# Kernel tuning notes

Measured on AMD Instinct MI355X. Metric: run time of the kernel, lower is better.

## Reference

```python
import jax, jax.numpy as jnp
import numpy as np

NUM_VARS = 50
EDGE_TYPES = 4
N_HID = 256
MSG_HID = N_HID // 8  # 32
IN_SIZE = 16
BATCH = 512
SKIP_FIRST = True

_adj = np.ones((NUM_VARS, NUM_VARS)) - np.eye(NUM_VARS)
SEND_EDGES, RECV_EDGES = np.where(_adj)
NUM_EDGES = SEND_EDGES.shape[0]  # 2450


def _lin(key, fan_in, fan_out):
    k1, k2 = jax.random.split(key)
    bound = 1.0 / np.sqrt(fan_in)
    w = jax.random.uniform(k1, (fan_in, fan_out), jnp.float32, -bound, bound)
    b = jax.random.uniform(k2, (fan_out,), jnp.float32, -bound, bound)
    return w, b


def setup_inputs() -> dict:
    key = jax.random.key(0)
    ks = jax.random.split(key, 10)
    inputs = jax.random.normal(ks[0], (BATCH, NUM_VARS, IN_SIZE), jnp.float32)
    edges = jax.random.uniform(ks[1], (BATCH, NUM_EDGES, EDGE_TYPES), jnp.float32)
    # per-edge-type message MLPs, stacked over edge-type axis
    f1 = [_lin(jax.random.fold_in(ks[2], i), 2 * IN_SIZE, MSG_HID) for i in range(EDGE_TYPES)]
    f2 = [_lin(jax.random.fold_in(ks[3], i), MSG_HID, MSG_HID) for i in range(EDGE_TYPES)]
    msg_fc1_w = jnp.stack([w for w, _ in f1]); msg_fc1_b = jnp.stack([b for _, b in f1])
    msg_fc2_w = jnp.stack([w for w, _ in f2]); msg_fc2_b = jnp.stack([b for _, b in f2])
    out_fc1_w, out_fc1_b = _lin(ks[4], IN_SIZE + MSG_HID, N_HID)
    out_fc2_w, out_fc2_b = _lin(ks[5], N_HID, N_HID)
    mu_w, mu_b = _lin(ks[6], N_HID, IN_SIZE)
    return dict(inputs=inputs, edges=edges,
                msg_fc1_w=msg_fc1_w, msg_fc1_b=msg_fc1_b,
                msg_fc2_w=msg_fc2_w, msg_fc2_b=msg_fc2_b,
                out_fc1_w=out_fc1_w, out_fc1_b=out_fc1_b,
                out_fc2_w=out_fc2_w, out_fc2_b=out_fc2_b,
                mu_w=mu_w, mu_b=mu_b)


def reference(inputs, edges, msg_fc1_w, msg_fc1_b, msg_fc2_w, msg_fc2_b,
              out_fc1_w, out_fc1_b, out_fc2_w, out_fc2_b, mu_w, mu_b):
    send = jnp.asarray(SEND_EDGES)
    recv = jnp.asarray(RECV_EDGES)
    # gather endpoints: [B, E, 2*in]
    pre_msg = jnp.concatenate([inputs[:, recv, :], inputs[:, send, :]], axis=-1)
    B = inputs.shape[0]
    all_msgs = jnp.zeros((B, NUM_EDGES, MSG_HID), inputs.dtype)
    start = 1 if SKIP_FIRST else 0
    for k in range(start, EDGE_TYPES):  # small fixed loop over edge types
        m = jax.nn.relu(pre_msg @ msg_fc1_w[k] + msg_fc1_b[k])
        m = jax.nn.relu(m @ msg_fc2_w[k] + msg_fc2_b[k])
        all_msgs = all_msgs + m * edges[:, :, k:k + 1]
    # scatter-sum edges -> receiver nodes (replaces dense edge2node_mat matmul)
    agg = jax.ops.segment_sum(jnp.swapaxes(all_msgs, 0, 1), recv,
                              num_segments=NUM_VARS)  # [V, B, H]
    agg = jnp.swapaxes(agg, 0, 1)  # [B, V, H]
    aug = jnp.concatenate([inputs, agg], axis=-1)
    pred = jax.nn.relu(aug @ out_fc1_w + out_fc1_b)
    pred = jax.nn.relu(pred @ out_fc2_w + out_fc2_b)
    mu = pred @ mu_w + mu_b  # eval mode: pi_action = mu (no rsample, dropout p=0)
    return (mu, pred)
```

## Files before the change

kernel.cpp:

```cpp
#include <hip/hip_runtime.h>
#include <hip/hip_bf16.h>
#include <hip/hip_fp16.h>

#define BATCHN 512
#define NV 50
#define NE 2450
#define INSZ 16
#define MH 32
#define NH 256

typedef short s16x8 __attribute__((ext_vector_type(8)));
typedef _Float16 f16x8 __attribute__((ext_vector_type(8)));
typedef float f32x4 __attribute__((ext_vector_type(4)));
typedef float f32x2 __attribute__((ext_vector_type(2)));

#define PRED_OFF (BATCHN * NV * INSZ)


__device__ __forceinline__ unsigned short f2bf(float x) {
  unsigned int u = __float_as_uint(x);
  unsigned int r = (u + 0x7fffu + ((u >> 16) & 1u)) >> 16;
  return (unsigned short)r;
}
__device__ __forceinline__ unsigned short f2h(float x) {
  return __half_as_ushort(__float2half(x));
}
__device__ __forceinline__ unsigned int pk2(float a, float b) {
  return (unsigned int)f2bf(a) | ((unsigned int)f2bf(b) << 16);
}
__device__ __forceinline__ unsigned int cvtpk(float lo, float hi) {
  unsigned int r;
  asm("v_cvt_pk_bf16_f32 %0, %1, %2" : "=v"(r) : "v"(lo), "v"(hi));
  return r;
}
__device__ __forceinline__ unsigned int pkmax0(unsigned int x, unsigned int z) {
  unsigned int r;
  asm("v_pk_max_i16 %0, %1, %2" : "=v"(r) : "v"(x), "v"(z));
  return r;
}
__device__ __forceinline__ unsigned int pkaddh(unsigned int a, unsigned int b) {
  unsigned int r;
  asm("v_pk_add_f16 %0, %1, %2" : "=v"(r) : "v"(a), "v"(b));
  return r;
}
__device__ __forceinline__ void pkfma(f32x2& acc, f32x2 a, f32x2 b) {
  asm("v_pk_fma_f32 %0, %1, %2, %0" : "+v"(acc) : "v"(a), "v"(b));
}

__global__ void k_tr(const float* __restrict__ w1, const float* __restrict__ w2,
                     const float* __restrict__ wo1, const float* __restrict__ wo2,
                     const float* __restrict__ wmu,
                     unsigned short* __restrict__ W2t, unsigned short* __restrict__ W1t,
                     unsigned short* __restrict__ Wt1sw, unsigned short* __restrict__ Wt2sw,
                     unsigned short* __restrict__ Wtmusw) {
  int idx = blockIdx.x * 256 + threadIdx.x;
  if (idx < 3072) {
    int c = idx & 31, h = (idx >> 5) & 31, kk = idx >> 10;
    W2t[idx] = f2h(w2[((kk + 1) * 32 + c) * 32 + h]);
  } else if (idx < 9216) {
    int j = idx - 3072;
    int k = j & 31, n = (j >> 5) & 31, kk = (j >> 10) % 3, half = j / 3072;
    W1t[j] = f2bf(k < 16 ? w1[((kk + 1) * 32 + half * 16 + k) * 32 + n] : 0.f);
  } else if (idx < 9216 + 16384) {
    int j = idx - 9216; int n = j & 255, kl = j >> 8;
    float v = kl < 48 ? wo1[kl * 256 + n] : 0.f;
    Wt1sw[n * 64 + (kl ^ ((n & 7) << 3))] = f2bf(v);
  } else if (idx < 9216 + 16384 + 65536) {
    int j = idx - (9216 + 16384);
    int c = j >> 14, r = j & 16383;
    int n = r & 255, kl = r >> 8;
    float v = wo2[(c * 64 + kl) * 256 + n];
    Wt2sw[(c * 256 + n) * 64 + (kl ^ ((n & 7) << 3))] = f2bf(v);
  } else if (idx < 9216 + 16384 + 65536 + 4096) {
    int j = idx - (9216 + 16384 + 65536);
    int n = j & 15, kl = j >> 4;
    Wtmusw[n * 256 + (kl ^ ((n & 7) << 3))] = f2bf(wmu[kl * 16 + n]);
  }
}

__global__ void __launch_bounds__(512, 4)
k_all(const float* __restrict__ inputs, const float* __restrict__ edges,
      const float* __restrict__ b1, const float* __restrict__ b2,
      const unsigned short* __restrict__ W1t, const unsigned short* __restrict__ W2t,
      const unsigned short* __restrict__ Wt1sw, const float* __restrict__ bo1,
      const unsigned short* __restrict__ Wt2sw, const float* __restrict__ bo2,
      const unsigned short* __restrict__ Wtmusw, const float* __restrict__ bmu,
      float* __restrict__ out) {
  __shared__ __align__(16) char smem[75776];
  unsigned short* S16 = (unsigned short*)(smem);
  unsigned short* R16 = (unsigned short*)(smem + 10400);
  float* E_lds = (float*)(smem + 20800);
  float* comb  = (float*)(smem + 10400);
  float* agg_l = (float*)(smem + 20800);
  unsigned short* aug = (unsigned short*)(smem);
  unsigned short* P1  = (unsigned short*)(smem + 9216);
  unsigned short* WB  = (unsigned short*)(smem + 43008);

  const int b   = blockIdx.x;
  const int tid = threadIdx.x;
  const int w   = tid >> 6;
  const int l   = tid & 63;
  const int grp = l >> 4;
  const int lm  = l & 15;
  const int jt  = w & 3;
  const int ih  = w >> 2;

  for (int x = tid; x < NV * 56; x += 512) {
    int i  = x / 56;
    int js = x - i * 56;
    float4 ev = make_float4(0.f, 0.f, 0.f, 0.f);
    if (js < NV && js != i) {
      int e = i * 49 + js - (js > i ? 1 : 0);
      ev = reinterpret_cast<const float4*>(edges)[b * NE + e];
    }
    int base = i * 168 + js;
    E_lds[base]       = ev.y;
    E_lds[base + 56]  = ev.z;
    E_lds[base + 112] = ev.w;
  }

  {
    const int half = w >> 2;
    const int mt4  = w & 3;
    int node  = mt4 * 16 + lm;
    int nodec = node < NV ? node : NV - 1;
    s16x8 af = {0, 0, 0, 0, 0, 0, 0, 0};
    if (grp < 2) {
      const float4* ip = reinterpret_cast<const float4*>(inputs) + (b * NV + nodec) * 4 + grp * 2;
      float4 x0 = ip[0], x1 = ip[1];
      union { unsigned int u[4]; s16x8 v; } U;
      U.u[0] = cvtpk(x0.x, x0.y); U.u[1] = cvtpk(x0.z, x0.w);
      U.u[2] = cvtpk(x1.x, x1.y); U.u[3] = cvtpk(x1.z, x1.w);
      af = U.v;
    }
    unsigned short* dst = half ? S16 : R16;
#pragma unroll
    for (int kk = 0; kk < 3; ++kk) {
#pragma unroll
      for (int nt = 0; nt < 2; ++nt) {
        int h = lm + 16 * nt;
        s16x8 bf = *reinterpret_cast<const s16x8*>(W1t + ((half * 3 + kk) * 32 + h) * 32 + grp * 8);
        f32x4 C;
        if (half == 0) { float bv = b1[(kk + 1) * 32 + h]; C = f32x4{bv, bv, bv, bv}; }
        else C = f32x4{0.f, 0.f, 0.f, 0.f};
        f32x4 o = __builtin_amdgcn_mfma_f32_16x16x32_bf16(af, bf, C, 0, 0, 0);
#pragma unroll
        for (int rr = 0; rr < 4; ++rr) {
          int n2 = mt4 * 16 + grp * 4 + rr;
          if (n2 < NV) dst[n2 * 104 + kk * 32 + h] = f2h(o[rr]);
        }
      }
    }
  }

  f16x8 Bf[3][2];
  f32x4 Cb[3][2];
#pragma unroll
  for (int kk = 0; kk < 3; ++kk)
#pragma unroll
    for (int nt = 0; nt < 2; ++nt) {
      int h = lm + 16 * nt;
      Bf[kk][nt] = *reinterpret_cast<const f16x8*>(W2t + (kk * 32 + h) * 32 + grp * 8);
      float bv = b2[(kk + 1) * 32 + h];
      Cb[kk][nt] = f32x4{bv, bv, bv, bv};
    }
  __syncthreads();

  unsigned int Rh[3][4];
  {
    int jrow = jt * 16 + lm;
    int jr   = jrow < NV ? jrow : NV - 1;
#pragma unroll
    for (int kk = 0; kk < 3; ++kk) {
      uint4 rv = *reinterpret_cast<const uint4*>(&R16[jr * 104 + kk * 32 + grp * 8]);
      Rh[kk][0] = rv.x; Rh[kk][1] = rv.y; Rh[kk][2] = rv.z; Rh[kk][3] = rv.w;
    }
  }
  __syncthreads();

  const int slot0 = jt * 16 + grp * 4;
  const int slot  = slot0 > 52 ? 52 : slot0;

  f32x2 acc0a = {0.f, 0.f}, acc0b = {0.f, 0.f};
  f32x2 acc1a = {0.f, 0.f}, acc1b = {0.f, 0.f};

#pragma unroll 4
  for (int i = ih; i < NV; i += 2) {
    const float* Eb = &E_lds[i * 168 + slot];
#pragma unroll
    for (int kk = 0; kk < 3; ++kk) {
      uint4 sv = *reinterpret_cast<const uint4*>(&S16[i * 104 + kk * 32 + grp * 8]);
      f32x4 ev = *reinterpret_cast<const f32x4*>(Eb + kk * 56);
      union { unsigned int u[4]; f16x8 v; } U;
      U.u[0] = pkmax0(pkaddh(Rh[kk][0], sv.x), 0u);
      U.u[1] = pkmax0(pkaddh(Rh[kk][1], sv.y), 0u);
      U.u[2] = pkmax0(pkaddh(Rh[kk][2], sv.z), 0u);
      U.u[3] = pkmax0(pkaddh(Rh[kk][3], sv.w), 0u);
      f32x4 d0 = __builtin_amdgcn_mfma_f32_16x16x32_f16(U.v, Bf[kk][0], Cb[kk][0], 0, 0, 0);
      f32x4 d1 = __builtin_amdgcn_mfma_f32_16x16x32_f16(U.v, Bf[kk][1], Cb[kk][1], 0, 0, 0);
      f32x2 ea = {ev[0], ev[1]}, eb = {ev[2], ev[3]};
      f32x2 r0a = {fmaxf(d0[0], 0.f), fmaxf(d0[1], 0.f)};
      f32x2 r0b = {fmaxf(d0[2], 0.f), fmaxf(d0[3], 0.f)};
      f32x2 r1a = {fmaxf(d1[0], 0.f), fmaxf(d1[1], 0.f)};
      f32x2 r1b = {fmaxf(d1[2], 0.f), fmaxf(d1[3], 0.f)};
      pkfma(acc0a, r0a, ea); pkfma(acc0b, r0b, eb);
      pkfma(acc1a, r1a, ea); pkfma(acc1b, r1b, eb);
    }
  }

  if (ih == 1) {
    int cbase = (jt * 64 + l) * 10;
    *reinterpret_cast<f32x2*>(&comb[cbase])     = acc0a;
    *reinterpret_cast<f32x2*>(&comb[cbase + 2]) = acc0b;
    *reinterpret_cast<f32x2*>(&comb[cbase + 4]) = acc1a;
    *reinterpret_cast<f32x2*>(&comb[cbase + 6]) = acc1b;
  }
  __syncthreads();
  if (ih == 0) {
    int cbase = (jt * 64 + l) * 10;
    acc0a += *reinterpret_cast<const f32x2*>(&comb[cbase]);
    acc0b += *reinterpret_cast<const f32x2*>(&comb[cbase + 2]);
    acc1a += *reinterpret_cast<const f32x2*>(&comb[cbase + 4]);
    acc1b += *reinterpret_cast<const f32x2*>(&comb[cbase + 6]);
    float a0v[4] = {acc0a[0], acc0a[1], acc0b[0], acc0b[1]};
    float a1v[4] = {acc1a[0], acc1a[1], acc1b[0], acc1b[1]};
#pragma unroll
    for (int rr = 0; rr < 4; ++rr) {
      int j = jt * 16 + grp * 4 + rr;
      if (j < NV) {
        agg_l[j * 32 + lm]      = a0v[rr];
        agg_l[j * 32 + 16 + lm] = a1v[rr];
      }
    }
  }
  __syncthreads();

  const int xo = (lm & 7) << 3;

  if (tid < 256) {
    int row = tid >> 2, q = tid & 3;
    uint2 u0; uint4 u1;
    if (row < NV) {
      float4 iv = reinterpret_cast<const float4*>(inputs)[(b * NV + row) * 4 + q];
      u0.x = pk2(iv.x, iv.y); u0.y = pk2(iv.z, iv.w);
      f32x4 a0 = *reinterpret_cast<const f32x4*>(&agg_l[row * 32 + q * 8]);
      f32x4 a1 = *reinterpret_cast<const f32x4*>(&agg_l[row * 32 + q * 8 + 4]);
      u1.x = pk2(a0[0], a0[1]); u1.y = pk2(a0[2], a0[3]);
      u1.z = pk2(a1[0], a1[1]); u1.w = pk2(a1[2], a1[3]);
    } else { u0.x = u0.y = 0u; u1.x = u1.y = u1.z = u1.w = 0u; }
    *reinterpret_cast<uint2*>(&aug[row * 72 + q * 4]) = u0;
    *reinterpret_cast<uint4*>(&aug[row * 72 + 16 + q * 8]) = u1;
    uint2 uz; uz.x = 0u; uz.y = 0u;
    *reinterpret_cast<uint2*>(&aug[row * 72 + 48 + q * 4]) = uz;
  }
  {
    const uint4* src = reinterpret_cast<const uint4*>(Wt1sw);
    for (int i2 = tid; i2 < 2048; i2 += 512) reinterpret_cast<uint4*>(WB)[i2] = src[i2];
  }
  __syncthreads();

  const int rowA  = 16 * jt + lm;
  const int kgrp  = grp * 8;
  const int rbase = 16 * jt + grp * 4;
  const int n0    = ih * 8;

  f32x4 acc1[8];
#pragma unroll
  for (int nt = 0; nt < 8; ++nt) acc1[nt] = f32x4{0.f, 0.f, 0.f, 0.f};
#pragma unroll
  for (int kc = 0; kc < 2; ++kc) {
    s16x8 af = *reinterpret_cast<const s16x8*>(&aug[rowA * 72 + kc * 32 + kgrp]);
#pragma unroll
    for (int nt = 0; nt < 8; ++nt) {
      int n = lm + 16 * (n0 + nt);
      s16x8 bf = *reinterpret_cast<const s16x8*>(&WB[n * 64 + ((kc * 32 + kgrp) ^ xo)]);
      acc1[nt] = __builtin_amdgcn_mfma_f32_16x16x32_bf16(af, bf, acc1[nt], 0, 0, 0);
    }
  }
#pragma unroll
  for (int nt = 0; nt < 8; ++nt) {
    int n = lm + 16 * (n0 + nt);
    float bias = bo1[n];
#pragma unroll
    for (int rr = 0; rr < 4; ++rr) {
      float v = acc1[nt][rr] + bias; v = v > 0.f ? v : 0.f;
      P1[(rbase + rr) * 264 + n] = f2bf(v);
    }
  }
  __syncthreads();

  f32x4 acc2[8];
#pragma unroll
  for (int nt = 0; nt < 8; ++nt) acc2[nt] = f32x4{0.f, 0.f, 0.f, 0.f};
  for (int c = 0; c < 4; ++c) {
    const uint4* src = reinterpret_cast<const uint4*>(Wt2sw + c * 16384);
    for (int i2 = tid; i2 < 2048; i2 += 512) reinterpret_cast<uint4*>(WB)[i2] = src[i2];
    __syncthreads();
#pragma unroll
    for (int kcl = 0; kcl < 2; ++kcl) {
      int kc = c * 2 + kcl;
      s16x8 af = *reinterpret_cast<const s16x8*>(&P1[rowA * 264 + kc * 32 + kgrp]);
#pragma unroll
      for (int nt = 0; nt < 8; ++nt) {
        int n = lm + 16 * (n0 + nt);
        s16x8 bf = *reinterpret_cast<const s16x8*>(&WB[n * 64 + ((kcl * 32 + kgrp) ^ xo)]);
        acc2[nt] = __builtin_amdgcn_mfma_f32_16x16x32_bf16(af, bf, acc2[nt], 0, 0, 0);
      }
    }
    __syncthreads();
  }
#pragma unroll
  for (int nt = 0; nt < 8; ++nt) {
    int n = lm + 16 * (n0 + nt);
    float bias = bo2[n];
#pragma unroll
    for (int rr = 0; rr < 4; ++rr) {
      int row = rbase + rr;
      float v = acc2[nt][rr] + bias; v = v > 0.f ? v : 0.f;
      if (row < NV) out[PRED_OFF + (b * NV + row) * 256 + n] = v;
      P1[row * 264 + n] = f2bf(v);
    }
  }
  reinterpret_cast<uint4*>(WB)[tid] = reinterpret_cast<const uint4*>(Wtmusw)[tid];
  __syncthreads();

  if (ih == 0) {
    f32x4 accm = {0.f, 0.f, 0.f, 0.f};
#pragma unroll
    for (int kc = 0; kc < 8; ++kc) {
      s16x8 af = *reinterpret_cast<const s16x8*>(&P1[rowA * 264 + kc * 32 + kgrp]);
      s16x8 bf = *reinterpret_cast<const s16x8*>(&WB[lm * 256 + ((kc * 32 + kgrp) ^ xo)]);
      accm = __builtin_amdgcn_mfma_f32_16x16x32_bf16(af, bf, accm, 0, 0, 0);
    }
    float bias = bmu[lm];
#pragma unroll
    for (int rr = 0; rr < 4; ++rr) {
      int row = rbase + rr;
      if (row < NV) out[(b * NV + row) * 16 + lm] = accm[rr] + bias;
    }
  }
}

extern "C" void kernel_launch(void* const* d_in, const int* in_sizes, int n_in,
                              void* d_out, int out_size, void* d_ws, size_t ws_size,
                              hipStream_t stream) {
  const float* inputs = (const float*)d_in[0];
  const float* edges  = (const float*)d_in[1];
  const float* w1     = (const float*)d_in[2];
  const float* b1     = (const float*)d_in[3];
  const float* w2     = (const float*)d_in[4];
  const float* b2     = (const float*)d_in[5];
  const float* wo1    = (const float*)d_in[6];
  const float* bo1    = (const float*)d_in[7];
  const float* wo2    = (const float*)d_in[8];
  const float* bo2    = (const float*)d_in[9];
  const float* wmu    = (const float*)d_in[10];
  const float* bmu    = (const float*)d_in[11];
  float* out = (float*)d_out;

  char* ws = (char*)d_ws;
  unsigned short* W2t    = (unsigned short*)(ws + 3276800);
  unsigned short* W1t    = (unsigned short*)(ws + 3282944);
  unsigned short* Wt1sw  = (unsigned short*)(ws + 3295232);
  unsigned short* Wt2sw  = (unsigned short*)(ws + 3328000);
  unsigned short* Wtmusw = (unsigned short*)(ws + 3459072);

  k_tr<<<372, 256, 0, stream>>>(w1, w2, wo1, wo2, wmu, W2t, W1t, Wt1sw, Wt2sw, Wtmusw);
  k_all<<<512, 512, 0, stream>>>(inputs, edges, b1, b2, W1t, W2t,
                                 Wt1sw, bo1, Wt2sw, bo2, Wtmusw, bmu, out);
}
```

Measured before the change: 49.42 us.

## Split each batch across two blocks by receiver half and shrink shared memory

Each block now handles 25 receiver nodes instead of all 50, so the grid grows to 512x2. The per-batch work is split across more blocks and the LDS footprint drops from about 74KB to about 39KB, with launch bounds raised so more blocks can be resident per CU. The edge-reduction loop is split four ways over senders instead of two. The output MLP weight staging is re-tiled into smaller K chunks, which adds more barriers. The sender-side first-layer projection is recomputed for all 50 nodes in both blocks, and weight loads double in total.

```diff
diff --git a/kernel.cpp b/kernel.cpp
--- a/kernel.cpp
+++ b/kernel.cpp
@@ -78,7 +78,7 @@
   }
 }
 
-__global__ void __launch_bounds__(512, 4)
+__global__ void __launch_bounds__(512, 8)
 k_all(const float* __restrict__ inputs, const float* __restrict__ edges,
       const float* __restrict__ b1, const float* __restrict__ b2,
       const unsigned short* __restrict__ W1t, const unsigned short* __restrict__ W2t,
@@ -86,43 +86,46 @@
       const unsigned short* __restrict__ Wt2sw, const float* __restrict__ bo2,
       const unsigned short* __restrict__ Wtmusw, const float* __restrict__ bmu,
       float* __restrict__ out) {
-  __shared__ __align__(16) char smem[75776];
+  __shared__ __align__(16) char smem[40352];
   unsigned short* S16 = (unsigned short*)(smem);
   unsigned short* R16 = (unsigned short*)(smem + 10400);
-  float* E_lds = (float*)(smem + 20800);
-  float* comb  = (float*)(smem + 10400);
-  float* agg_l = (float*)(smem + 20800);
-  unsigned short* aug = (unsigned short*)(smem);
-  unsigned short* P1  = (unsigned short*)(smem + 9216);
-  unsigned short* WB  = (unsigned short*)(smem + 43008);
-
-  const int b   = blockIdx.x;
-  const int tid = threadIdx.x;
-  const int w   = tid >> 6;
-  const int l   = tid & 63;
-  const int grp = l >> 4;
-  const int lm  = l & 15;
-  const int jt  = w & 3;
-  const int ih  = w >> 2;
-
-  for (int x = tid; x < NV * 56; x += 512) {
-    int i  = x / 56;
-    int js = x - i * 56;
+  float* E_lds = (float*)(smem + 17056);
+  float* comb  = (float*)(smem);
+  float* agg_l = (float*)(smem + 36256);
+  unsigned short* WB  = (unsigned short*)(smem);
+  unsigned short* aug = (unsigned short*)(smem + 18432);
+  unsigned short* P1  = (unsigned short*)(smem + 23040);
+
+  const int b     = blockIdx.x;
+  const int jh    = blockIdx.y;
+  const int jbase = jh * 25;
+  const int tid   = threadIdx.x;
+  const int w     = tid >> 6;
+  const int l     = tid & 63;
+  const int grp   = l >> 4;
+  const int lm    = l & 15;
+  const int jt    = w & 1;
+  const int ih    = w >> 1;
+
+  for (int x = tid; x < NV * 32; x += 512) {
+    int i  = x >> 5;
+    int js = x & 31;
+    int gj = jbase + js;
     float4 ev = make_float4(0.f, 0.f, 0.f, 0.f);
-    if (js < NV && js != i) {
-      int e = i * 49 + js - (js > i ? 1 : 0);
+    if (js < 25 && gj != i) {
+      int e = i * 49 + gj - (gj > i ? 1 : 0);
       ev = reinterpret_cast<const float4*>(edges)[b * NE + e];
     }
-    int base = i * 168 + js;
-    E_lds[base]       = ev.y;
-    E_lds[base + 56]  = ev.z;
-    E_lds[base + 112] = ev.w;
-  }
-
-  {
-    const int half = w >> 2;
-    const int mt4  = w & 3;
-    int node  = mt4 * 16 + lm;
+    int base = i * 96 + js;
+    E_lds[base]      = ev.y;
+    E_lds[base + 32] = ev.z;
+    E_lds[base + 64] = ev.w;
+  }
+
+  if (w < 6) {
+    const int half = (w < 4) ? 1 : 0;
+    const int mt4  = (w < 4) ? w : (w - 4);
+    int node  = (w < 4) ? (mt4 * 16 + lm) : (jbase + mt4 * 16 + lm);
     int nodec = node < NV ? node : NV - 1;
     s16x8 af = {0, 0, 0, 0, 0, 0, 0, 0};
     if (grp < 2) {
@@ -147,57 +150,59 @@
 #pragma unroll
         for (int rr = 0; rr < 4; ++rr) {
           int n2 = mt4 * 16 + grp * 4 + rr;
-          if (n2 < NV) dst[n2 * 104 + kk * 32 + h] = f2h(o[rr]);
+          if (half == 0) {
+            dst[n2 * 104 + kk * 32 + h] = f2h(o[rr]);
+          } else if (n2 < NV) {
+            dst[n2 * 104 + kk * 32 + h] = f2h(o[rr]);
+          }
         }
       }
     }
   }
 
   f16x8 Bf[3][2];
-  f32x4 Cb[3][2];
+  float cb[3][2];
 #pragma unroll
   for (int kk = 0; kk < 3; ++kk)
 #pragma unroll
     for (int nt = 0; nt < 2; ++nt) {
       int h = lm + 16 * nt;
       Bf[kk][nt] = *reinterpret_cast<const f16x8*>(W2t + (kk * 32 + h) * 32 + grp * 8);
-      float bv = b2[(kk + 1) * 32 + h];
-      Cb[kk][nt] = f32x4{bv, bv, bv, bv};
+      cb[kk][nt] = b2[(kk + 1) * 32 + h];
     }
   __syncthreads();
 
   unsigned int Rh[3][4];
   {
-    int jrow = jt * 16 + lm;
-    int jr   = jrow < NV ? jrow : NV - 1;
+    int jr = jt * 16 + lm;
 #pragma unroll
     for (int kk = 0; kk < 3; ++kk) {
       uint4 rv = *reinterpret_cast<const uint4*>(&R16[jr * 104 + kk * 32 + grp * 8]);
       Rh[kk][0] = rv.x; Rh[kk][1] = rv.y; Rh[kk][2] = rv.z; Rh[kk][3] = rv.w;
     }
   }
-  __syncthreads();
 
   const int slot0 = jt * 16 + grp * 4;
-  const int slot  = slot0 > 52 ? 52 : slot0;
 
   f32x2 acc0a = {0.f, 0.f}, acc0b = {0.f, 0.f};
   f32x2 acc1a = {0.f, 0.f}, acc1b = {0.f, 0.f};
 
 #pragma unroll 4
-  for (int i = ih; i < NV; i += 2) {
-    const float* Eb = &E_lds[i * 168 + slot];
+  for (int i = ih; i < NV; i += 4) {
+    const float* Eb = &E_lds[i * 96 + slot0];
 #pragma unroll
     for (int kk = 0; kk < 3; ++kk) {
       uint4 sv = *reinterpret_cast<const uint4*>(&S16[i * 104 + kk * 32 + grp * 8]);
-      f32x4 ev = *reinterpret_cast<const f32x4*>(Eb + kk * 56);
+      f32x4 ev = *reinterpret_cast<const f32x4*>(Eb + kk * 32);
       union { unsigned int u[4]; f16x8 v; } U;
       U.u[0] = pkmax0(pkaddh(Rh[kk][0], sv.x), 0u);
       U.u[1] = pkmax0(pkaddh(Rh[kk][1], sv.y), 0u);
       U.u[2] = pkmax0(pkaddh(Rh[kk][2], sv.z), 0u);
       U.u[3] = pkmax0(pkaddh(Rh[kk][3], sv.w), 0u);
-      f32x4 d0 = __builtin_amdgcn_mfma_f32_16x16x32_f16(U.v, Bf[kk][0], Cb[kk][0], 0, 0, 0);
-      f32x4 d1 = __builtin_amdgcn_mfma_f32_16x16x32_f16(U.v, Bf[kk][1], Cb[kk][1], 0, 0, 0);
+      f32x4 C0 = f32x4{cb[kk][0], cb[kk][0], cb[kk][0], cb[kk][0]};
+      f32x4 C1 = f32x4{cb[kk][1], cb[kk][1], cb[kk][1], cb[kk][1]};
+      f32x4 d0 = __builtin_amdgcn_mfma_f32_16x16x32_f16(U.v, Bf[kk][0], C0, 0, 0, 0);
+      f32x4 d1 = __builtin_amdgcn_mfma_f32_16x16x32_f16(U.v, Bf[kk][1], C1, 0, 0, 0);
       f32x2 ea = {ev[0], ev[1]}, eb = {ev[2], ev[3]};
       f32x2 r0a = {fmaxf(d0[0], 0.f), fmaxf(d0[1], 0.f)};
       f32x2 r0b = {fmaxf(d0[2], 0.f), fmaxf(d0[3], 0.f)};
@@ -207,9 +212,10 @@
       pkfma(acc1a, r1a, ea); pkfma(acc1b, r1b, eb);
     }
   }
-
-  if (ih == 1) {
-    int cbase = (jt * 64 + l) * 10;
+  __syncthreads();
+
+  if (ih != 0) {
+    int cbase = (((ih - 1) * 2 + jt) * 64 + l) * 8;
     *reinterpret_cast<f32x2*>(&comb[cbase])     = acc0a;
     *reinterpret_cast<f32x2*>(&comb[cbase + 2]) = acc0b;
     *reinterpret_cast<f32x2*>(&comb[cbase + 4]) = acc1a;
@@ -217,17 +223,20 @@
   }
   __syncthreads();
   if (ih == 0) {
-    int cbase = (jt * 64 + l) * 10;
-    acc0a += *reinterpret_cast<const f32x2*>(&comb[cbase]);
-    acc0b += *reinterpret_cast<const f32x2*>(&comb[cbase + 2]);
-    acc1a += *reinterpret_cast<const f32x2*>(&comb[cbase + 4]);
-    acc1b += *reinterpret_cast<const f32x2*>(&comb[cbase + 6]);
+#pragma unroll
+    for (int p = 0; p < 3; ++p) {
+      int cbase = ((p * 2 + jt) * 64 + l) * 8;
+      acc0a += *reinterpret_cast<const f32x2*>(&comb[cbase]);
+      acc0b += *reinterpret_cast<const f32x2*>(&comb[cbase + 2]);
+      acc1a += *reinterpret_cast<const f32x2*>(&comb[cbase + 4]);
+      acc1b += *reinterpret_cast<const f32x2*>(&comb[cbase + 6]);
+    }
     float a0v[4] = {acc0a[0], acc0a[1], acc0b[0], acc0b[1]};
     float a1v[4] = {acc1a[0], acc1a[1], acc1b[0], acc1b[1]};
 #pragma unroll
     for (int rr = 0; rr < 4; ++rr) {
       int j = jt * 16 + grp * 4 + rr;
-      if (j < NV) {
+      if (j < 25) {
         agg_l[j * 32 + lm]      = a0v[rr];
         agg_l[j * 32 + 16 + lm] = a1v[rr];
       }
@@ -235,13 +244,17 @@
   }
   __syncthreads();
 
-  const int xo = (lm & 7) << 3;
-
-  if (tid < 256) {
+  const int rowt = w & 1;
+  const int nq   = w >> 1;
+  const int rowA = rowt * 16 + lm;
+  const int kgrp = grp * 8;
+  const int rbase = rowt * 16 + grp * 4;
+
+  if (tid < 128) {
     int row = tid >> 2, q = tid & 3;
     uint2 u0; uint4 u1;
-    if (row < NV) {
-      float4 iv = reinterpret_cast<const float4*>(inputs)[(b * NV + row) * 4 + q];
+    if (row < 25) {
+      float4 iv = reinterpret_cast<const float4*>(inputs)[(b * NV + jbase + row) * 4 + q];
       u0.x = pk2(iv.x, iv.y); u0.y = pk2(iv.z, iv.w);
       f32x4 a0 = *reinterpret_cast<const f32x4*>(&agg_l[row * 32 + q * 8]);
       f32x4 a1 = *reinterpret_cast<const f32x4*>(&agg_l[row * 32 + q * 8 + 4]);
@@ -253,33 +266,30 @@
     uint2 uz; uz.x = 0u; uz.y = 0u;
     *reinterpret_cast<uint2*>(&aug[row * 72 + 48 + q * 4]) = uz;
   }
-  {
-    const uint4* src = reinterpret_cast<const uint4*>(Wt1sw);
-    for (int i2 = tid; i2 < 2048; i2 += 512) reinterpret_cast<uint4*>(WB)[i2] = src[i2];
-  }
-  __syncthreads();
-
-  const int rowA  = 16 * jt + lm;
-  const int kgrp  = grp * 8;
-  const int rbase = 16 * jt + grp * 4;
-  const int n0    = ih * 8;
-
-  f32x4 acc1[8];
-#pragma unroll
-  for (int nt = 0; nt < 8; ++nt) acc1[nt] = f32x4{0.f, 0.f, 0.f, 0.f};
-#pragma unroll
-  for (int kc = 0; kc < 2; ++kc) {
-    s16x8 af = *reinterpret_cast<const s16x8*>(&aug[rowA * 72 + kc * 32 + kgrp]);
-#pragma unroll
-    for (int nt = 0; nt < 8; ++nt) {
-      int n = lm + 16 * (n0 + nt);
-      s16x8 bf = *reinterpret_cast<const s16x8*>(&WB[n * 64 + ((kc * 32 + kgrp) ^ xo)]);
+
+  f32x4 acc1[4];
+#pragma unroll
+  for (int nt = 0; nt < 4; ++nt) acc1[nt] = f32x4{0.f, 0.f, 0.f, 0.f};
+  for (int c = 0; c < 2; ++c) {
+    for (int x = tid; x < 2048; x += 512) {
+      int n = x >> 3, q = x & 7;
+      int soff = (c * 32 + q * 4) ^ ((n & 7) << 3);
+      uint2 v = *reinterpret_cast<const uint2*>(Wt1sw + n * 64 + soff);
+      *reinterpret_cast<uint2*>(reinterpret_cast<unsigned int*>(WB) + n * 18 + q * 2) = v;
+    }
+    __syncthreads();
+    s16x8 af = *reinterpret_cast<const s16x8*>(&aug[rowA * 72 + c * 32 + kgrp]);
+#pragma unroll
+    for (int nt = 0; nt < 4; ++nt) {
+      int n = lm + 16 * (nq * 4 + nt);
+      s16x8 bf = *reinterpret_cast<const s16x8*>(&WB[n * 36 + grp * 8]);
       acc1[nt] = __builtin_amdgcn_mfma_f32_16x16x32_bf16(af, bf, acc1[nt], 0, 0, 0);
     }
-  }
-#pragma unroll
-  for (int nt = 0; nt < 8; ++nt) {
-    int n = lm + 16 * (n0 + nt);
+    __syncthreads();
+  }
+#pragma unroll
+  for (int nt = 0; nt < 4; ++nt) {
+    int n = lm + 16 * (nq * 4 + nt);
     float bias = bo1[n];
 #pragma unroll
     for (int rr = 0; rr < 4; ++rr) {
@@ -287,44 +297,46 @@
       P1[(rbase + rr) * 264 + n] = f2bf(v);
     }
   }
-  __syncthreads();
-
-  f32x4 acc2[8];
-#pragma unroll
-  for (int nt = 0; nt < 8; ++nt) acc2[nt] = f32x4{0.f, 0.f, 0.f, 0.f};
-  for (int c = 0; c < 4; ++c) {
-    const uint4* src = reinterpret_cast<const uint4*>(Wt2sw + c * 16384);
-    for (int i2 = tid; i2 < 2048; i2 += 512) reinterpret_cast<uint4*>(WB)[i2] = src[i2];
+
+  f32x4 acc2[4];
+#pragma unroll
+  for (int nt = 0; nt < 4; ++nt) acc2[nt] = f32x4{0.f, 0.f, 0.f, 0.f};
+  for (int c = 0; c < 8; ++c) {
+    const unsigned short* src = Wt2sw + (c >> 1) * 16384;
+    int khalf = c & 1;
+    for (int x = tid; x < 2048; x += 512) {
+      int n = x >> 3, q = x & 7;
+      int soff = (khalf * 32 + q * 4) ^ ((n & 7) << 3);
+      uint2 v = *reinterpret_cast<const uint2*>(src + n * 64 + soff);
+      *reinterpret_cast<uint2*>(reinterpret_cast<unsigned int*>(WB) + n * 18 + q * 2) = v;
+    }
     __syncthreads();
-#pragma unroll
-    for (int kcl = 0; kcl < 2; ++kcl) {
-      int kc = c * 2 + kcl;
-      s16x8 af = *reinterpret_cast<const s16x8*>(&P1[rowA * 264 + kc * 32 + kgrp]);
-#pragma unroll
-      for (int nt = 0; nt < 8; ++nt) {
-        int n = lm + 16 * (n0 + nt);
-        s16x8 bf = *reinterpret_cast<const s16x8*>(&WB[n * 64 + ((kcl * 32 + kgrp) ^ xo)]);
-        acc2[nt] = __builtin_amdgcn_mfma_f32_16x16x32_bf16(af, bf, acc2[nt], 0, 0, 0);
-      }
+    s16x8 af = *reinterpret_cast<const s16x8*>(&P1[rowA * 264 + c * 32 + kgrp]);
+#pragma unroll
+    for (int nt = 0; nt < 4; ++nt) {
+      int n = lm + 16 * (nq * 4 + nt);
+      s16x8 bf = *reinterpret_cast<const s16x8*>(&WB[n * 36 + grp * 8]);
+      acc2[nt] = __builtin_amdgcn_mfma_f32_16x16x32_bf16(af, bf, acc2[nt], 0, 0, 0);
     }
     __syncthreads();
   }
 #pragma unroll
-  for (int nt = 0; nt < 8; ++nt) {
-    int n = lm + 16 * (n0 + nt);
+  for (int nt = 0; nt < 4; ++nt) {
+    int n = lm + 16 * (nq * 4 + nt);
     float bias = bo2[n];
 #pragma unroll
     for (int rr = 0; rr < 4; ++rr) {
       int row = rbase + rr;
       float v = acc2[nt][rr] + bias; v = v > 0.f ? v : 0.f;
-      if (row < NV) out[PRED_OFF + (b * NV + row) * 256 + n] = v;
+      if (row < 25) out[PRED_OFF + (b * NV + jbase + row) * 256 + n] = v;
       P1[row * 264 + n] = f2bf(v);
     }
   }
   reinterpret_cast<uint4*>(WB)[tid] = reinterpret_cast<const uint4*>(Wtmusw)[tid];
   __syncthreads();
 
-  if (ih == 0) {
+  if (nq == 0) {
+    const int xo = (lm & 7) << 3;
     f32x4 accm = {0.f, 0.f, 0.f, 0.f};
 #pragma unroll
     for (int kc = 0; kc < 8; ++kc) {
@@ -336,7 +348,7 @@
 #pragma unroll
     for (int rr = 0; rr < 4; ++rr) {
       int row = rbase + rr;
-      if (row < NV) out[(b * NV + row) * 16 + lm] = accm[rr] + bias;
+      if (row < 25) out[(b * NV + jbase + row) * 16 + lm] = accm[rr] + bias;
     }
   }
 }
@@ -366,6 +378,6 @@
   unsigned short* Wtmusw = (unsigned short*)(ws + 3459072);
 
   k_tr<<<372, 256, 0, stream>>>(w1, w2, wo1, wo2, wmu, W2t, W1t, Wt1sw, Wt2sw, Wtmusw);
-  k_all<<<512, 512, 0, stream>>>(inputs, edges, b1, b2, W1t, W2t,
-                                 Wt1sw, bo1, Wt2sw, bo2, Wtmusw, bmu, out);
-}
+  k_all<<<dim3(512, 2), 512, 0, stream>>>(inputs, edges, b1, b2, W1t, W2t,
+                                          Wt1sw, bo1, Wt2sw, bo2, Wtmusw, bmu, out);
+}
```

Result: slower. 135.0 us (+173.2%).

## Load output-MLP weights as pre-packed MFMA fragments directly from global memory

Applied to the files above, without the earlier changes.

The prep kernel now writes out_fc1, out_fc2 and mu weights in per-lane MFMA B-fragment order, so each lane reads its 8 bf16 values with one contiguous 16-byte global load. This removes the LDS staging of weight chunks and the barriers around each of the four fc2 chunk loads. The LDS footprint drops from about 74KB to 53KB, which may allow more resident blocks per CU. In exchange, every block reads the weights from L2/global with per-wave latency instead of sharing one staged copy through LDS.

```diff
diff --git a/kernel.cpp b/kernel.cpp
--- a/kernel.cpp
+++ b/kernel.cpp
@@ -51,8 +51,8 @@
                      const float* __restrict__ wo1, const float* __restrict__ wo2,
                      const float* __restrict__ wmu,
                      unsigned short* __restrict__ W2t, unsigned short* __restrict__ W1t,
-                     unsigned short* __restrict__ Wt1sw, unsigned short* __restrict__ Wt2sw,
-                     unsigned short* __restrict__ Wtmusw) {
+                     unsigned short* __restrict__ W1f, unsigned short* __restrict__ W2f,
+                     unsigned short* __restrict__ Wmuf) {
   int idx = blockIdx.x * 256 + threadIdx.x;
   if (idx < 3072) {
     int c = idx & 31, h = (idx >> 5) & 31, kk = idx >> 10;
@@ -62,19 +62,23 @@
     int k = j & 31, n = (j >> 5) & 31, kk = (j >> 10) % 3, half = j / 3072;
     W1t[j] = f2bf(k < 16 ? w1[((kk + 1) * 32 + half * 16 + k) * 32 + n] : 0.f);
   } else if (idx < 9216 + 16384) {
-    int j = idx - 9216; int n = j & 255, kl = j >> 8;
-    float v = kl < 48 ? wo1[kl * 256 + n] : 0.f;
-    Wt1sw[n * 64 + (kl ^ ((n & 7) << 3))] = f2bf(v);
+    int j = idx - 9216;
+    int f = j >> 9, r = j & 511, lane = r >> 3, e = r & 7;
+    int n = (lane & 15) + 16 * (f >> 1);
+    int k = (f & 1) * 32 + ((lane >> 4) << 3) + e;
+    W1f[j] = f2bf(k < 48 ? wo1[k * 256 + n] : 0.f);
   } else if (idx < 9216 + 16384 + 65536) {
     int j = idx - (9216 + 16384);
-    int c = j >> 14, r = j & 16383;
-    int n = r & 255, kl = r >> 8;
-    float v = wo2[(c * 64 + kl) * 256 + n];
-    Wt2sw[(c * 256 + n) * 64 + (kl ^ ((n & 7) << 3))] = f2bf(v);
+    int f = j >> 9, r = j & 511, lane = r >> 3, e = r & 7;
+    int n = (lane & 15) + 16 * (f >> 3);
+    int k = (f & 7) * 32 + ((lane >> 4) << 3) + e;
+    W2f[j] = f2bf(wo2[k * 256 + n]);
   } else if (idx < 9216 + 16384 + 65536 + 4096) {
     int j = idx - (9216 + 16384 + 65536);
-    int n = j & 15, kl = j >> 4;
-    Wtmusw[n * 256 + (kl ^ ((n & 7) << 3))] = f2bf(wmu[kl * 16 + n]);
+    int f = j >> 9, r = j & 511, lane = r >> 3, e = r & 7;
+    int n = lane & 15;
+    int k = f * 32 + ((lane >> 4) << 3) + e;
+    Wmuf[j] = f2bf(wmu[k * 16 + n]);
   }
 }
 
@@ -82,19 +86,18 @@
 k_all(const float* __restrict__ inputs, const float* __restrict__ edges,
       const float* __restrict__ b1, const float* __restrict__ b2,
       const unsigned short* __restrict__ W1t, const unsigned short* __restrict__ W2t,
-      const unsigned short* __restrict__ Wt1sw, const float* __restrict__ bo1,
-      const unsigned short* __restrict__ Wt2sw, const float* __restrict__ bo2,
-      const unsigned short* __restrict__ Wtmusw, const float* __restrict__ bmu,
+      const unsigned short* __restrict__ W1f, const float* __restrict__ bo1,
+      const unsigned short* __restrict__ W2f, const float* __restrict__ bo2,
+      const unsigned short* __restrict__ Wmuf, const float* __restrict__ bmu,
       float* __restrict__ out) {
-  __shared__ __align__(16) char smem[75776];
+  __shared__ __align__(16) char smem[54400];
   unsigned short* S16 = (unsigned short*)(smem);
   unsigned short* R16 = (unsigned short*)(smem + 10400);
   float* E_lds = (float*)(smem + 20800);
   float* comb  = (float*)(smem + 10400);
-  float* agg_l = (float*)(smem + 20800);
   unsigned short* aug = (unsigned short*)(smem);
   unsigned short* P1  = (unsigned short*)(smem + 9216);
-  unsigned short* WB  = (unsigned short*)(smem + 43008);
+  float* agg_l = (float*)(smem + 43008);
 
   const int b   = blockIdx.x;
   const int tid = threadIdx.x;
@@ -235,8 +238,6 @@
   }
   __syncthreads();
 
-  const int xo = (lm & 7) << 3;
-
   if (tid < 256) {
     int row = tid >> 2, q = tid & 3;
     uint2 u0; uint4 u1;
@@ -253,10 +254,6 @@
     uint2 uz; uz.x = 0u; uz.y = 0u;
     *reinterpret_cast<uint2*>(&aug[row * 72 + 48 + q * 4]) = uz;
   }
-  {
-    const uint4* src = reinterpret_cast<const uint4*>(Wt1sw);
-    for (int i2 = tid; i2 < 2048; i2 += 512) reinterpret_cast<uint4*>(WB)[i2] = src[i2];
-  }
   __syncthreads();
 
   const int rowA  = 16 * jt + lm;
@@ -272,8 +269,8 @@
     s16x8 af = *reinterpret_cast<const s16x8*>(&aug[rowA * 72 + kc * 32 + kgrp]);
 #pragma unroll
     for (int nt = 0; nt < 8; ++nt) {
-      int n = lm + 16 * (n0 + nt);
-      s16x8 bf = *reinterpret_cast<const s16x8*>(&WB[n * 64 + ((kc * 32 + kgrp) ^ xo)]);
+      int f = (n0 + nt) * 2 + kc;
+      s16x8 bf = *reinterpret_cast<const s16x8*>(W1f + (f * 64 + l) * 8);
       acc1[nt] = __builtin_amdgcn_mfma_f32_16x16x32_bf16(af, bf, acc1[nt], 0, 0, 0);
     }
   }
@@ -292,23 +289,18 @@
   f32x4 acc2[8];
 #pragma unroll
   for (int nt = 0; nt < 8; ++nt) acc2[nt] = f32x4{0.f, 0.f, 0.f, 0.f};
-  for (int c = 0; c < 4; ++c) {
-    const uint4* src = reinterpret_cast<const uint4*>(Wt2sw + c * 16384);
-    for (int i2 = tid; i2 < 2048; i2 += 512) reinterpret_cast<uint4*>(WB)[i2] = src[i2];
-    __syncthreads();
-#pragma unroll
-    for (int kcl = 0; kcl < 2; ++kcl) {
-      int kc = c * 2 + kcl;
-      s16x8 af = *reinterpret_cast<const s16x8*>(&P1[rowA * 264 + kc * 32 + kgrp]);
-#pragma unroll
-      for (int nt = 0; nt < 8; ++nt) {
-        int n = lm + 16 * (n0 + nt);
-        s16x8 bf = *reinterpret_cast<const s16x8*>(&WB[n * 64 + ((kcl * 32 + kgrp) ^ xo)]);
-        acc2[nt] = __builtin_amdgcn_mfma_f32_16x16x32_bf16(af, bf, acc2[nt], 0, 0, 0);
-      }
-    }
-    __syncthreads();
-  }
+#pragma unroll 2
+  for (int kc = 0; kc < 8; ++kc) {
+    s16x8 af = *reinterpret_cast<const s16x8*>(&P1[rowA * 264 + kc * 32 + kgrp]);
+#pragma unroll
+    for (int nt = 0; nt < 8; ++nt) {
+      int f = (n0 + nt) * 8 + kc;
+      s16x8 bf = *reinterpret_cast<const s16x8*>(W2f + (f * 64 + l) * 8);
+      acc2[nt] = __builtin_amdgcn_mfma_f32_16x16x32_bf16(af, bf, acc2[nt], 0, 0, 0);
+    }
+  }
+  __syncthreads();
+
 #pragma unroll
   for (int nt = 0; nt < 8; ++nt) {
     int n = lm + 16 * (n0 + nt);
@@ -321,7 +313,6 @@
       P1[row * 264 + n] = f2bf(v);
     }
   }
-  reinterpret_cast<uint4*>(WB)[tid] = reinterpret_cast<const uint4*>(Wtmusw)[tid];
   __syncthreads();
 
   if (ih == 0) {
@@ -329,7 +320,7 @@
 #pragma unroll
     for (int kc = 0; kc < 8; ++kc) {
       s16x8 af = *reinterpret_cast<const s16x8*>(&P1[rowA * 264 + kc * 32 + kgrp]);
-      s16x8 bf = *reinterpret_cast<const s16x8*>(&WB[lm * 256 + ((kc * 32 + kgrp) ^ xo)]);
+      s16x8 bf = *reinterpret_cast<const s16x8*>(Wmuf + (kc * 64 + l) * 8);
       accm = __builtin_amdgcn_mfma_f32_16x16x32_bf16(af, bf, accm, 0, 0, 0);
     }
     float bias = bmu[lm];
@@ -359,13 +350,13 @@
   float* out = (float*)d_out;
 
   char* ws = (char*)d_ws;
-  unsigned short* W2t    = (unsigned short*)(ws + 3276800);
-  unsigned short* W1t    = (unsigned short*)(ws + 3282944);
-  unsigned short* Wt1sw  = (unsigned short*)(ws + 3295232);
-  unsigned short* Wt2sw  = (unsigned short*)(ws + 3328000);
-  unsigned short* Wtmusw = (unsigned short*)(ws + 3459072);
-
-  k_tr<<<372, 256, 0, stream>>>(w1, w2, wo1, wo2, wmu, W2t, W1t, Wt1sw, Wt2sw, Wtmusw);
+  unsigned short* W2t  = (unsigned short*)(ws + 3276800);
+  unsigned short* W1t  = (unsigned short*)(ws + 3282944);
+  unsigned short* W1f  = (unsigned short*)(ws + 3295232);
+  unsigned short* W2f  = (unsigned short*)(ws + 3328000);
+  unsigned short* Wmuf = (unsigned short*)(ws + 3459072);
+
+  k_tr<<<372, 256, 0, stream>>>(w1, w2, wo1, wo2, wmu, W2t, W1t, W1f, W2f, Wmuf);
   k_all<<<512, 512, 0, stream>>>(inputs, edges, b1, b2, W1t, W2t,
-                                 Wt1sw, bo1, Wt2sw, bo2, Wtmusw, bmu, out);
-}
+                                 W1f, bo1, W2f, bo2, Wmuf, bmu, out);
+}
```

After: 56.24 us. 13.8% more time.
